# Kernel optimization log

Measured on AMD Instinct MI355X. Metric: run time of the kernel, lower is better.

Reference implementation:

```python
import jax, jax.numpy as jnp
import numpy as np

EXPANSION_K = 5
N_CENTERS = 8192
DIM = 512
BATCH = 4096


def setup_inputs() -> dict:
    key = jax.random.key(0)
    k1, k2, k3 = jax.random.split(key, 3)
    z = jax.random.normal(k1, (BATCH, DIM), dtype=jnp.float32)
    # learned PMField parameters: center positions and gravitational masses
    centers = jax.random.normal(k2, (N_CENTERS, DIM), dtype=jnp.float32)
    mus = jax.random.uniform(k3, (N_CENTERS,), dtype=jnp.float32, minval=0.1, maxval=1.0)
    return {"z": z, "centers": centers, "mus": mus}


def reference(z, centers, mus):
    # --- compute_center_attractions ---
    # torch.cdist(z, centers) -> Euclidean distances (B, N), computed GEMM-style
    sq = (
        jnp.sum(z * z, axis=-1, keepdims=True)          # (B, 1)
        + jnp.sum(centers * centers, axis=-1)[None, :]   # (1, N)
        - 2.0 * (z @ centers.T)                          # (B, N)
    )
    dists = jnp.sqrt(jnp.maximum(sq, 0.0))
    attractions = mus[None, :] / (dists ** 2 + 1e-6)     # (B, N)

    # --- expand_query ---
    top_vals, top_idx = jax.lax.top_k(attractions, EXPANSION_K)  # (B, k)
    weights = jax.nn.softmax(top_vals, axis=1)                    # (B, k)
    expanded_centers = centers[top_idx]                           # gather -> (B, k, D)
    comb = jnp.einsum("bkd,bk->bd", expanded_centers, weights)   # weighted center combine
    expanded_z = 0.7 * z + 0.3 * comb                             # (B, D)
    return expanded_z, attractions
```

## Files before the change

### kernel.cpp

```cpp
#include <hip/hip_runtime.h>
#include <math.h>

#define BATCH 4096
#define NC    8192
#define DIM   512
#define KEXP  5
#define NCAND 10

using bf16x8 = __attribute__((ext_vector_type(8))) short;
using f32x4  = __attribute__((ext_vector_type(4))) float;
typedef unsigned long long u64;

__device__ unsigned short g_zbf[BATCH * DIM];
__device__ unsigned short g_cbf[NC * DIM];
__device__ float g_z2[BATCH];
__device__ float g_c2[NC];

__device__ __forceinline__ unsigned short rtne_bf16(float f) {
  unsigned u = __float_as_uint(f);
  u += 0x7FFFu + ((u >> 16) & 1u);
  return (unsigned short)(u >> 16);
}

__device__ __forceinline__ void gload16(const void* g, void* l) {
  __builtin_amdgcn_global_load_lds(
      (const __attribute__((address_space(1))) void*)g,
      (__attribute__((address_space(3))) void*)l, 16, 0, 0);
}

__global__ __launch_bounds__(256) void convert_kernel(const float* __restrict__ z,
                                                      const float* __restrict__ c) {
  const size_t i = ((size_t)blockIdx.x * 256 + threadIdx.x) * 8;
  const size_t zn = (size_t)BATCH * DIM;
  const float* src;
  unsigned short* dst;
  size_t off;
  if (i < zn) { src = z; dst = g_zbf; off = i; }
  else        { src = c; dst = g_cbf; off = i - zn; }
  float4 a = *(const float4*)(src + off);
  float4 b = *(const float4*)(src + off + 4);
  uint4 o;
  o.x = (unsigned)rtne_bf16(a.x) | ((unsigned)rtne_bf16(a.y) << 16);
  o.y = (unsigned)rtne_bf16(a.z) | ((unsigned)rtne_bf16(a.w) << 16);
  o.z = (unsigned)rtne_bf16(b.x) | ((unsigned)rtne_bf16(b.y) << 16);
  o.w = (unsigned)rtne_bf16(b.z) | ((unsigned)rtne_bf16(b.w) << 16);
  *(uint4*)(dst + off) = o;
}

__global__ __launch_bounds__(128) void norms_kernel(const float* __restrict__ z,
                                                    const float* __restrict__ c) {
  int row = blockIdx.x;
  const float* src;
  float* dst;
  if (row < BATCH) { src = z + (size_t)row * DIM; dst = g_z2 + row; }
  else             { src = c + (size_t)(row - BATCH) * DIM; dst = g_c2 + (row - BATCH); }
  int t = threadIdx.x;
  float4 v = ((const float4*)src)[t];
  double acc = (double)v.x * v.x + (double)v.y * v.y + (double)v.z * v.z + (double)v.w * v.w;
#pragma unroll
  for (int off = 32; off > 0; off >>= 1) acc += __shfl_down(acc, off);
  __shared__ double wsum[2];
  if ((t & 63) == 0) wsum[t >> 6] = acc;
  __syncthreads();
  if (t == 0) *dst = (float)(wsum[0] + wsum[1]);
}

#define BM  128
#define BN  128
#define BKK 64

__global__ __launch_bounds__(256) void attr_bf16(const float* __restrict__ mus,
                                                 float* __restrict__ att) {
  __shared__ __align__(16) unsigned short Ah[BM * BKK];
  __shared__ __align__(16) unsigned short Bh[BM * BKK];

  const int tid  = threadIdx.x;
  const int lane = tid & 63;
  const int wid  = tid >> 6;
  const int wm   = wid >> 1;
  const int wn   = wid & 1;

  const int flat = blockIdx.y * gridDim.x + blockIdx.x;
  const int swz  = (flat & 7) * 256 + (flat >> 3);
  const int col0 = (swz & 63) * BN;
  const int row0 = (swz >> 6) * BM;

  f32x4 acc[4][4] = {};

  const unsigned short* Ag = g_zbf + (size_t)row0 * DIM;
  const unsigned short* Bg = g_cbf + (size_t)col0 * DIM;

  const int crow = lane >> 3;
  const int gsw  = (lane & 7) ^ crow;

  for (int k0 = 0; k0 < DIM; k0 += BKK) {
#pragma unroll
    for (int j = 0; j < 4; ++j) {
      const int base_row = (wid * 4 + j) * 8;
      const int r = base_row + crow;
      gload16(Ag + (size_t)r * DIM + k0 + gsw * 8, Ah + base_row * 64);
      gload16(Bg + (size_t)r * DIM + k0 + gsw * 8, Bh + base_row * 64);
    }
    __syncthreads();

#pragma unroll
    for (int kk = 0; kk < 2; ++kk) {
      bf16x8 fa[4], fb[4];
#pragma unroll
      for (int i = 0; i < 4; ++i) {
        const int r = wm * 64 + i * 16 + (lane & 15);
        const int g = (kk * 4 + (lane >> 4)) ^ (r & 7);
        fa[i] = *(const bf16x8*)((const char*)Ah + r * 128 + g * 16);
      }
#pragma unroll
      for (int j2 = 0; j2 < 4; ++j2) {
        const int r = wn * 64 + j2 * 16 + (lane & 15);
        const int g = (kk * 4 + (lane >> 4)) ^ (r & 7);
        fb[j2] = *(const bf16x8*)((const char*)Bh + r * 128 + g * 16);
      }
#pragma unroll
      for (int i = 0; i < 4; ++i)
#pragma unroll
        for (int j2 = 0; j2 < 4; ++j2)
          acc[i][j2] = __builtin_amdgcn_mfma_f32_16x16x32_bf16(fa[i], fb[j2], acc[i][j2], 0, 0, 0);
    }
    __syncthreads();
  }

#pragma unroll
  for (int i = 0; i < 4; ++i) {
    const int mrow = row0 + wm * 64 + i * 16 + (lane >> 4) * 4;
    float zz[4];
#pragma unroll
    for (int r = 0; r < 4; ++r) zz[r] = g_z2[mrow + r];
#pragma unroll
    for (int j = 0; j < 4; ++j) {
      const int gc = col0 + wn * 64 + j * 16 + (lane & 15);
      const float cc = g_c2[gc];
      const float mu = mus[gc];
#pragma unroll
      for (int r = 0; r < 4; ++r) {
        float t   = __fadd_rn(zz[r], cc);
        float sq  = __fsub_rn(t, __fmul_rn(2.0f, acc[i][j][r]));
        float d   = sqrtf(fmaxf(sq, 0.0f));
        float den = __fadd_rn(__fmul_rn(d, d), 1e-6f);
        att[(size_t)(mrow + r) * NC + gc] = __fdiv_rn(mu, den);
      }
    }
  }
}

__global__ __launch_bounds__(256, 4) void topk_kernel(const float* __restrict__ att,
                                                      const float* __restrict__ z,
                                                      const float* __restrict__ centers,
                                                      const float* __restrict__ mus,
                                                      float* __restrict__ out) {
  __shared__ int selLds[4][16];
  const int lane = threadIdx.x & 63;
  const int wv   = threadIdx.x >> 6;
  const int row  = blockIdx.x * 4 + wv;
  const float4* arow4 = (const float4*)(att + (size_t)row * NC);

  u64 k[8][4];
#pragma unroll
  for (int c = 0; c < 8; ++c) {
#pragma unroll
    for (int j = 0; j < 4; ++j) k[c][j] = 0ull;
#pragma unroll
    for (int q = 0; q < 4; ++q) {
      float4 v4 = arow4[c * 256 + q * 64 + lane];
      const unsigned ib = (unsigned)(c * 1024 + q * 256 + lane * 4);
      const float vv[4] = {v4.x, v4.y, v4.z, v4.w};
#pragma unroll
      for (int e = 0; e < 4; ++e) {
        u64 nk = ((u64)__float_as_uint(vv[e]) << 32) | (u64)(0xFFFFFFFFu - (ib + e));
        bool g0 = nk > k[c][0], g1 = nk > k[c][1], g2 = nk > k[c][2], g3 = nk > k[c][3];
        u64 t0 = k[c][0], t1 = k[c][1], t2 = k[c][2];
        k[c][0] = g0 ? nk : k[c][0];
        k[c][1] = g0 ? t0 : (g1 ? nk : k[c][1]);
        k[c][2] = g1 ? t1 : (g2 ? nk : k[c][2]);
        k[c][3] = g2 ? t2 : (g3 ? nk : k[c][3]);
      }
    }
  }

  for (int it = 0; it < NCAND; ++it) {
    u64 b = k[0][0];
#pragma unroll
    for (int c = 1; c < 8; ++c) b = (k[c][0] > b) ? k[c][0] : b;
#pragma unroll
    for (int off = 32; off > 0; off >>= 1) {
      u64 o = __shfl_xor(b, off);
      b = (o > b) ? o : b;
    }
    if (lane == 0) selLds[wv][it] = (int)(0xFFFFFFFFu - (unsigned)(b & 0xFFFFFFFFu));
#pragma unroll
    for (int c = 0; c < 8; ++c) {
      bool hit = (k[c][0] == b);
      k[c][0] = hit ? k[c][1] : k[c][0];
      k[c][1] = hit ? k[c][2] : k[c][1];
      k[c][2] = hit ? k[c][3] : k[c][2];
      k[c][3] = hit ? 0ull    : k[c][3];
    }
  }

  const float* zrow = z + (size_t)row * DIM;
  const int d0 = lane * 8;
  const float4 za = *(const float4*)(zrow + d0);
  const float4 zb = *(const float4*)(zrow + d0 + 4);
  const float myz2 = g_z2[row];

  double p[NCAND];
  int cidx[NCAND];
#pragma unroll
  for (int c = 0; c < NCAND; ++c) {
    cidx[c] = selLds[wv][c];
    const float* cp = centers + (size_t)cidx[c] * DIM + d0;
    float4 ca = *(const float4*)(cp);
    float4 cb = *(const float4*)(cp + 4);
    p[c] = (double)za.x * ca.x + (double)za.y * ca.y +
           (double)za.z * ca.z + (double)za.w * ca.w +
           (double)zb.x * cb.x + (double)zb.y * cb.y +
           (double)zb.z * cb.z + (double)zb.w * cb.w;
  }
#pragma unroll
  for (int off = 32; off > 0; off >>= 1) {
#pragma unroll
    for (int c = 0; c < NCAND; ++c) p[c] += __shfl_xor(p[c], off);
  }

  float exv[NCAND];
#pragma unroll
  for (int c = 0; c < NCAND; ++c) {
    const int ci = cidx[c];
    float dotf = (float)p[c];
    float t   = __fadd_rn(myz2, g_c2[ci]);
    float sq  = __fsub_rn(t, __fmul_rn(2.0f, dotf));
    float d   = sqrtf(fmaxf(sq, 0.0f));
    float den = __fadd_rn(__fmul_rn(d, d), 1e-6f);
    exv[c] = __fdiv_rn(mus[ci], den);
  }

  unsigned used = 0;
  float tv[KEXP]; int tix[KEXP];
#pragma unroll
  for (int s = 0; s < KEXP; ++s) {
    float bv = -INFINITY; int bi = 0x7FFFFFFF; int bc = 0;
#pragma unroll
    for (int c = 0; c < NCAND; ++c) {
      bool ok = (used & (1u << c)) == 0;
      if (ok && (exv[c] > bv || (exv[c] == bv && cidx[c] < bi))) {
        bv = exv[c]; bi = cidx[c]; bc = c;
      }
    }
    used |= (1u << bc);
    tv[s] = bv; tix[s] = bi;
  }

  float m = tv[0];
  float w[KEXP];
  float s = 0.0f;
#pragma unroll
  for (int kk = 0; kk < KEXP; ++kk) { w[kk] = expf(tv[kk] - m); s += w[kk]; }
#pragma unroll
  for (int kk = 0; kk < KEXP; ++kk) w[kk] /= s;

  float comb[8] = {0, 0, 0, 0, 0, 0, 0, 0};
#pragma unroll
  for (int kk = 0; kk < KEXP; ++kk) {
    const float* cp = centers + (size_t)tix[kk] * DIM + d0;
    float4 a = *(const float4*)(cp);
    float4 bq = *(const float4*)(cp + 4);
    comb[0] += w[kk] * a.x;  comb[1] += w[kk] * a.y;
    comb[2] += w[kk] * a.z;  comb[3] += w[kk] * a.w;
    comb[4] += w[kk] * bq.x; comb[5] += w[kk] * bq.y;
    comb[6] += w[kk] * bq.z; comb[7] += w[kk] * bq.w;
  }
  const float zv[8] = {za.x, za.y, za.z, za.w, zb.x, zb.y, zb.z, zb.w};
  float o[8];
#pragma unroll
  for (int e = 0; e < 8; ++e)
    o[e] = __fadd_rn(__fmul_rn(0.7f, zv[e]), __fmul_rn(0.3f, comb[e]));
  *(float4*)(out + (size_t)row * DIM + d0)     = *(float4*)&o[0];
  *(float4*)(out + (size_t)row * DIM + d0 + 4) = *(float4*)&o[4];
}

extern "C" void kernel_launch(void* const* d_in, const int* in_sizes, int n_in,
                              void* d_out, int out_size, void* d_ws, size_t ws_size,
                              hipStream_t stream) {
  const float* z       = (const float*)d_in[0];
  const float* centers = (const float*)d_in[1];
  const float* mus     = (const float*)d_in[2];
  float* out      = (float*)d_out;
  float* expanded = out;
  float* att      = out + (size_t)BATCH * DIM;

  convert_kernel<<<(BATCH + NC) * DIM / (256 * 8), 256, 0, stream>>>(z, centers);
  norms_kernel<<<BATCH + NC, 128, 0, stream>>>(z, centers);
  dim3 grid(NC / BN, BATCH / BM);
  attr_bf16<<<grid, 256, 0, stream>>>(mus, att);
  topk_kernel<<<BATCH / 4, 256, 0, stream>>>(att, z, centers, mus, expanded);
}
```

Measured before the change: 155.1 us.

## Double-buffer GEMM LDS tiles, remap blocks per XCD, vectorize attraction stores

The bf16 MFMA distance GEMM now uses double-buffered 32-wide K stages, so the next tile's global-to-LDS loads are issued while the current tile is consumed. That removes one barrier per step. The grid is a 1D launch with a new XCD-aware block mapping that groups row tiles per XCD for L2 reuse. Operand roles are swapped in the MFMA so each lane holds four consecutive columns, which allows float4 stores of attractions and float4 loads of the norms and mus. The smaller K step means more iterations and barriers, and the new swizzle pattern must stay free of LDS bank conflicts.

```diff
diff --git a/kernel.cpp b/kernel.cpp
--- a/kernel.cpp
+++ b/kernel.cpp
@@ -67,87 +67,100 @@
 
 #define BM  128
 #define BN  128
-#define BKK 64
 
 __global__ __launch_bounds__(256) void attr_bf16(const float* __restrict__ mus,
                                                  float* __restrict__ att) {
-  __shared__ __align__(16) unsigned short Ah[BM * BKK];
-  __shared__ __align__(16) unsigned short Bh[BM * BKK];
+  __shared__ __align__(16) unsigned short Ab[2][BM * 32];
+  __shared__ __align__(16) unsigned short Bb[2][BM * 32];
 
   const int tid  = threadIdx.x;
   const int lane = tid & 63;
-  const int wid  = tid >> 6;
-  const int wm   = wid >> 1;
-  const int wn   = wid & 1;
-
-  const int flat = blockIdx.y * gridDim.x + blockIdx.x;
-  const int swz  = (flat & 7) * 256 + (flat >> 3);
-  const int col0 = (swz & 63) * BN;
-  const int row0 = (swz >> 6) * BM;
-
-  f32x4 acc[4][4] = {};
+  const int wv   = tid >> 6;
+  const int wm   = wv >> 1;
+  const int wn   = wv & 1;
+
+  const int flat = blockIdx.x;
+  const int xcd  = flat & 7;
+  const int t    = flat >> 3;
+  const int row0 = (xcd * 4 + (t & 3)) * BM;
+  const int col0 = (t >> 2) * BN;
 
   const unsigned short* Ag = g_zbf + (size_t)row0 * DIM;
   const unsigned short* Bg = g_cbf + (size_t)col0 * DIM;
 
-  const int crow = lane >> 3;
-  const int gsw  = (lane & 7) ^ crow;
-
-  for (int k0 = 0; k0 < DIM; k0 += BKK) {
+  const int srow = wv * 16 + (lane >> 2);
+  const int sg   = (lane & 3) ^ ((lane >> 3) & 3);
+
+  const int q  = lane >> 4;
+  const int gq = q ^ (((lane & 15) >> 1) & 3);
+  const int l15 = lane & 15;
+
+  f32x4 acc[4][4] = {};
+
+#define STAGE(S, B)                                                         \
+  {                                                                         \
+    const int k0_ = (S) * 32;                                               \
+    _Pragma("unroll")                                                       \
+    for (int inst = 0; inst < 2; ++inst) {                                  \
+      const int r_ = inst * 64 + srow;                                      \
+      gload16(Ag + (size_t)r_ * DIM + k0_ + sg * 8,                         \
+              &Ab[B][(inst * 64 + wv * 16) * 32]);                          \
+      gload16(Bg + (size_t)r_ * DIM + k0_ + sg * 8,                         \
+              &Bb[B][(inst * 64 + wv * 16) * 32]);                          \
+    }                                                                       \
+  }
+
+  STAGE(0, 0);
+  __syncthreads();
+
+  for (int s = 0; s < 16; ++s) {
+    const int cur = s & 1;
+    if (s < 15) STAGE(s + 1, cur ^ 1);
+
+    bf16x8 fa[4], fb[4];
+#pragma unroll
+    for (int i = 0; i < 4; ++i) {
+      const int r = wm * 64 + i * 16 + l15;
+      fa[i] = *(const bf16x8*)((const char*)&Ab[cur][0] + r * 64 + gq * 16);
+    }
 #pragma unroll
     for (int j = 0; j < 4; ++j) {
-      const int base_row = (wid * 4 + j) * 8;
-      const int r = base_row + crow;
-      gload16(Ag + (size_t)r * DIM + k0 + gsw * 8, Ah + base_row * 64);
-      gload16(Bg + (size_t)r * DIM + k0 + gsw * 8, Bh + base_row * 64);
-    }
+      const int r = wn * 64 + j * 16 + l15;
+      fb[j] = *(const bf16x8*)((const char*)&Bb[cur][0] + r * 64 + gq * 16);
+    }
+#pragma unroll
+    for (int j = 0; j < 4; ++j)
+#pragma unroll
+      for (int i = 0; i < 4; ++i)
+        acc[j][i] = __builtin_amdgcn_mfma_f32_16x16x32_bf16(fb[j], fa[i], acc[j][i], 0, 0, 0);
     __syncthreads();
-
-#pragma unroll
-    for (int kk = 0; kk < 2; ++kk) {
-      bf16x8 fa[4], fb[4];
-#pragma unroll
-      for (int i = 0; i < 4; ++i) {
-        const int r = wm * 64 + i * 16 + (lane & 15);
-        const int g = (kk * 4 + (lane >> 4)) ^ (r & 7);
-        fa[i] = *(const bf16x8*)((const char*)Ah + r * 128 + g * 16);
-      }
-#pragma unroll
-      for (int j2 = 0; j2 < 4; ++j2) {
-        const int r = wn * 64 + j2 * 16 + (lane & 15);
-        const int g = (kk * 4 + (lane >> 4)) ^ (r & 7);
-        fb[j2] = *(const bf16x8*)((const char*)Bh + r * 128 + g * 16);
-      }
-#pragma unroll
-      for (int i = 0; i < 4; ++i)
-#pragma unroll
-        for (int j2 = 0; j2 < 4; ++j2)
-          acc[i][j2] = __builtin_amdgcn_mfma_f32_16x16x32_bf16(fa[i], fb[j2], acc[i][j2], 0, 0, 0);
-    }
-    __syncthreads();
   }
 
 #pragma unroll
   for (int i = 0; i < 4; ++i) {
-    const int mrow = row0 + wm * 64 + i * 16 + (lane >> 4) * 4;
-    float zz[4];
-#pragma unroll
-    for (int r = 0; r < 4; ++r) zz[r] = g_z2[mrow + r];
+    const int ar = row0 + wm * 64 + i * 16 + l15;
+    const float zz = g_z2[ar];
+    float* dst = att + (size_t)ar * NC;
 #pragma unroll
     for (int j = 0; j < 4; ++j) {
-      const int gc = col0 + wn * 64 + j * 16 + (lane & 15);
-      const float cc = g_c2[gc];
-      const float mu = mus[gc];
+      const int gc0 = col0 + wn * 64 + j * 16 + q * 4;
+      const float4 cc = *(const float4*)&g_c2[gc0];
+      const float4 mu = *(const float4*)&mus[gc0];
+      const float ccv[4] = {cc.x, cc.y, cc.z, cc.w};
+      const float muv[4] = {mu.x, mu.y, mu.z, mu.w};
+      float o[4];
 #pragma unroll
       for (int r = 0; r < 4; ++r) {
-        float t   = __fadd_rn(zz[r], cc);
-        float sq  = __fsub_rn(t, __fmul_rn(2.0f, acc[i][j][r]));
+        float tt  = __fadd_rn(zz, ccv[r]);
+        float sq  = __fsub_rn(tt, __fmul_rn(2.0f, acc[j][i][r]));
         float d   = sqrtf(fmaxf(sq, 0.0f));
         float den = __fadd_rn(__fmul_rn(d, d), 1e-6f);
-        att[(size_t)(mrow + r) * NC + gc] = __fdiv_rn(mu, den);
+        o[r] = __fdiv_rn(muv[r], den);
       }
-    }
-  }
+      *(float4*)(dst + gc0) = *(const float4*)o;
+    }
+  }
+#undef STAGE
 }
 
 __global__ __launch_bounds__(256, 4) void topk_kernel(const float* __restrict__ att,
@@ -167,9 +180,9 @@
 #pragma unroll
     for (int j = 0; j < 4; ++j) k[c][j] = 0ull;
 #pragma unroll
-    for (int q = 0; q < 4; ++q) {
-      float4 v4 = arow4[c * 256 + q * 64 + lane];
-      const unsigned ib = (unsigned)(c * 1024 + q * 256 + lane * 4);
+    for (int qq = 0; qq < 4; ++qq) {
+      float4 v4 = arow4[c * 256 + qq * 64 + lane];
+      const unsigned ib = (unsigned)(c * 1024 + qq * 256 + lane * 4);
       const float vv[4] = {v4.x, v4.y, v4.z, v4.w};
 #pragma unroll
       for (int e = 0; e < 4; ++e) {
@@ -297,7 +310,6 @@
 
   convert_kernel<<<(BATCH + NC) * DIM / (256 * 8), 256, 0, stream>>>(z, centers);
   norms_kernel<<<BATCH + NC, 128, 0, stream>>>(z, centers);
-  dim3 grid(NC / BN, BATCH / BM);
-  attr_bf16<<<grid, 256, 0, stream>>>(mus, att);
+  attr_bf16<<<(BATCH / BM) * (NC / BN), 256, 0, stream>>>(mus, att);
   topk_kernel<<<BATCH / 4, 256, 0, stream>>>(att, z, centers, mus, expanded);
 }
```

After: 178.2 us. 1.15x slower.

## Split GEMM epilogue into fragment-layout dump plus coalesced attraction stream kernel

Applied to the files above, without the earlier changes.

The GEMM now writes raw MFMA accumulator fragments contiguously to a scratch buffer. A new row-wise kernel reads them back, applies the distance and attraction math, and writes the output with fully coalesced float4 stores. The aim is to remove the scattered 4-byte stores in the GEMM epilogue. The row-norm computation is also folded into the bf16 convert kernel via a wave shuffle reduction, which drops one launch. The cost is an extra 128 MB write and read through the scratch buffer.

```diff
diff --git a/kernel.cpp b/kernel.cpp
--- a/kernel.cpp
+++ b/kernel.cpp
@@ -15,6 +15,7 @@
 __device__ unsigned short g_cbf[NC * DIM];
 __device__ float g_z2[BATCH];
 __device__ float g_c2[NC];
+__device__ float g_dots[(size_t)BATCH * NC];
 
 __device__ __forceinline__ unsigned short rtne_bf16(float f) {
   unsigned u = __float_as_uint(f);
@@ -34,9 +35,10 @@
   const size_t zn = (size_t)BATCH * DIM;
   const float* src;
   unsigned short* dst;
+  float* ndst;
   size_t off;
-  if (i < zn) { src = z; dst = g_zbf; off = i; }
-  else        { src = c; dst = g_cbf; off = i - zn; }
+  if (i < zn) { src = z; dst = g_zbf; ndst = g_z2; off = i; }
+  else        { src = c; dst = g_cbf; ndst = g_c2; off = i - zn; }
   float4 a = *(const float4*)(src + off);
   float4 b = *(const float4*)(src + off + 4);
   uint4 o;
@@ -45,32 +47,19 @@
   o.z = (unsigned)rtne_bf16(b.x) | ((unsigned)rtne_bf16(b.y) << 16);
   o.w = (unsigned)rtne_bf16(b.z) | ((unsigned)rtne_bf16(b.w) << 16);
   *(uint4*)(dst + off) = o;
-}
-
-__global__ __launch_bounds__(128) void norms_kernel(const float* __restrict__ z,
-                                                    const float* __restrict__ c) {
-  int row = blockIdx.x;
-  const float* src;
-  float* dst;
-  if (row < BATCH) { src = z + (size_t)row * DIM; dst = g_z2 + row; }
-  else             { src = c + (size_t)(row - BATCH) * DIM; dst = g_c2 + (row - BATCH); }
-  int t = threadIdx.x;
-  float4 v = ((const float4*)src)[t];
-  double acc = (double)v.x * v.x + (double)v.y * v.y + (double)v.z * v.z + (double)v.w * v.w;
-#pragma unroll
-  for (int off = 32; off > 0; off >>= 1) acc += __shfl_down(acc, off);
-  __shared__ double wsum[2];
-  if ((t & 63) == 0) wsum[t >> 6] = acc;
-  __syncthreads();
-  if (t == 0) *dst = (float)(wsum[0] + wsum[1]);
+
+  double s = (double)a.x * a.x + (double)a.y * a.y + (double)a.z * a.z + (double)a.w * a.w +
+             (double)b.x * b.x + (double)b.y * b.y + (double)b.z * b.z + (double)b.w * b.w;
+#pragma unroll
+  for (int sh = 32; sh > 0; sh >>= 1) s += __shfl_xor(s, sh);
+  if ((threadIdx.x & 63) == 0) ndst[off / DIM] = (float)s;
 }
 
 #define BM  128
 #define BN  128
 #define BKK 64
 
-__global__ __launch_bounds__(256) void attr_bf16(const float* __restrict__ mus,
-                                                 float* __restrict__ att) {
+__global__ __launch_bounds__(256) void gemm_dots() {
   __shared__ __align__(16) unsigned short Ah[BM * BKK];
   __shared__ __align__(16) unsigned short Bh[BM * BKK];
 
@@ -80,10 +69,12 @@
   const int wm   = wid >> 1;
   const int wn   = wid & 1;
 
-  const int flat = blockIdx.y * gridDim.x + blockIdx.x;
+  const int flat = blockIdx.x;
   const int swz  = (flat & 7) * 256 + (flat >> 3);
-  const int col0 = (swz & 63) * BN;
-  const int row0 = (swz >> 6) * BM;
+  const int tile_c = swz & 63;
+  const int tile_r = swz >> 6;
+  const int col0 = tile_c * BN;
+  const int row0 = tile_r * BM;
 
   f32x4 acc[4][4] = {};
 
@@ -119,34 +110,62 @@
         fb[j2] = *(const bf16x8*)((const char*)Bh + r * 128 + g * 16);
       }
 #pragma unroll
-      for (int i = 0; i < 4; ++i)
-#pragma unroll
-        for (int j2 = 0; j2 < 4; ++j2)
-          acc[i][j2] = __builtin_amdgcn_mfma_f32_16x16x32_bf16(fa[i], fb[j2], acc[i][j2], 0, 0, 0);
+      for (int j2 = 0; j2 < 4; ++j2)
+#pragma unroll
+        for (int i = 0; i < 4; ++i)
+          acc[j2][i] = __builtin_amdgcn_mfma_f32_16x16x32_bf16(fb[j2], fa[i], acc[j2][i], 0, 0, 0);
     }
     __syncthreads();
   }
 
-#pragma unroll
-  for (int i = 0; i < 4; ++i) {
-    const int mrow = row0 + wm * 64 + i * 16 + (lane >> 4) * 4;
-    float zz[4];
-#pragma unroll
-    for (int r = 0; r < 4; ++r) zz[r] = g_z2[mrow + r];
-#pragma unroll
-    for (int j = 0; j < 4; ++j) {
-      const int gc = col0 + wn * 64 + j * 16 + (lane & 15);
-      const float cc = g_c2[gc];
-      const float mu = mus[gc];
-#pragma unroll
-      for (int r = 0; r < 4; ++r) {
-        float t   = __fadd_rn(zz[r], cc);
-        float sq  = __fsub_rn(t, __fmul_rn(2.0f, acc[i][j][r]));
-        float d   = sqrtf(fmaxf(sq, 0.0f));
-        float den = __fadd_rn(__fmul_rn(d, d), 1e-6f);
-        att[(size_t)(mrow + r) * NC + gc] = __fdiv_rn(mu, den);
-      }
-    }
+  float* dbase = g_dots + (size_t)(tile_r * 64 + tile_c) * 16384 + (size_t)wid * 4096 + lane * 4;
+#pragma unroll
+  for (int j = 0; j < 4; ++j)
+#pragma unroll
+    for (int i = 0; i < 4; ++i)
+      *(f32x4*)(dbase + (j * 4 + i) * 256) = acc[j][i];
+}
+
+__global__ __launch_bounds__(256) void att_stream(const float* __restrict__ mus,
+                                                  float* __restrict__ att) {
+  const int ar  = blockIdx.x;
+  const int tid = threadIdx.x;
+  const int tile_r = ar >> 7;
+  const int a   = ar & 127;
+  const int wm  = a >> 6;
+  const int i_  = (a >> 4) & 3;
+  const int l15 = a & 15;
+  const float zz = g_z2[ar];
+  float* dst = att + (size_t)ar * NC;
+
+#pragma unroll
+  for (int k = 0; k < 8; ++k) {
+    const int f  = k * 256 + tid;
+    const int cg = f * 4;
+    const int tile_c = cg >> 7;
+    const int c  = cg & 127;
+    const int wn = c >> 6;
+    const int j_ = (c >> 4) & 3;
+    const int q  = (c >> 2) & 3;
+    const size_t off = (size_t)(tile_r * 64 + tile_c) * 16384 +
+                       (size_t)((wm * 2 + wn) * 16 + j_ * 4 + i_) * 256 +
+                       (q * 16 + l15) * 4;
+    const float4 dv = *(const float4*)(g_dots + off);
+    const float4 cc = *(const float4*)(g_c2 + cg);
+    const float4 mu = *(const float4*)(mus + cg);
+    const float dvv[4] = {dv.x, dv.y, dv.z, dv.w};
+    const float ccv[4] = {cc.x, cc.y, cc.z, cc.w};
+    const float muv[4] = {mu.x, mu.y, mu.z, mu.w};
+    float o[4];
+#pragma unroll
+    for (int r = 0; r < 4; ++r) {
+      float tt  = __fadd_rn(zz, ccv[r]);
+      float sq  = __fsub_rn(tt, __fmul_rn(2.0f, dvv[r]));
+      float d   = sqrtf(fmaxf(sq, 0.0f));
+      float den = __fadd_rn(__fmul_rn(d, d), 1e-6f);
+      o[r] = __fdiv_rn(muv[r], den);
+    }
+    *(float4*)(dst + cg) = *(const float4*)o;
   }
 }
 
@@ -167,9 +186,9 @@
 #pragma unroll
     for (int j = 0; j < 4; ++j) k[c][j] = 0ull;
 #pragma unroll
-    for (int q = 0; q < 4; ++q) {
-      float4 v4 = arow4[c * 256 + q * 64 + lane];
-      const unsigned ib = (unsigned)(c * 1024 + q * 256 + lane * 4);
+    for (int qq = 0; qq < 4; ++qq) {
+      float4 v4 = arow4[c * 256 + qq * 64 + lane];
+      const unsigned ib = (unsigned)(c * 1024 + qq * 256 + lane * 4);
       const float vv[4] = {v4.x, v4.y, v4.z, v4.w};
 #pragma unroll
       for (int e = 0; e < 4; ++e) {
@@ -257,11 +276,11 @@
     tv[s] = bv; tix[s] = bi;
   }
 
-  float m = tv[0];
+  float mm = tv[0];
   float w[KEXP];
   float s = 0.0f;
 #pragma unroll
-  for (int kk = 0; kk < KEXP; ++kk) { w[kk] = expf(tv[kk] - m); s += w[kk]; }
+  for (int kk = 0; kk < KEXP; ++kk) { w[kk] = expf(tv[kk] - mm); s += w[kk]; }
 #pragma unroll
   for (int kk = 0; kk < KEXP; ++kk) w[kk] /= s;
 
@@ -296,8 +315,7 @@
   float* att      = out + (size_t)BATCH * DIM;
 
   convert_kernel<<<(BATCH + NC) * DIM / (256 * 8), 256, 0, stream>>>(z, centers);
-  norms_kernel<<<BATCH + NC, 128, 0, stream>>>(z, centers);
-  dim3 grid(NC / BN, BATCH / BM);
-  attr_bf16<<<grid, 256, 0, stream>>>(mus, att);
+  gemm_dots<<<(BATCH / BM) * (NC / BN), 256, 0, stream>>>();
+  att_stream<<<BATCH, 256, 0, stream>>>(mus, att);
   topk_kernel<<<BATCH / 4, 256, 0, stream>>>(att, z, centers, mus, expanded);
 }
```

New measurement: 307.4 us. +98.2%, slower.
